# Optimization experiments

Hardware: AMD Instinct MI355X
Metric: run time of the kernel (lower is better)

The kernel has to match this reference:

```python
import jax, jax.numpy as jnp
import numpy as np

B, S, H = 1, 2048, 4096
NH, NKV, HD = 32, 8, 128
GROUPS = NH // NKV  # 4
THETA = 10000.0
NEG = -1e9


def setup_inputs() -> dict:
    key = jax.random.key(0)
    k1, k2, k3 = jax.random.split(key, 3)
    hidden_states = jax.random.normal(k1, (B, S, H), dtype=jnp.float32)
    w_qkv = jax.random.normal(k2, (H, (NH + 2 * NKV) * HD), dtype=jnp.float32) * 0.02
    w_o = jax.random.normal(k3, (NH * HD, H), dtype=jnp.float32) * 0.02
    causal = jnp.tril(jnp.ones((S, S), dtype=bool))
    attention_mask = jnp.where(causal, 0.0, NEG).astype(jnp.float32)[None, None]  # [1,1,S,S]
    return {"hidden_states": hidden_states, "w_qkv": w_qkv, "w_o": w_o,
            "attention_mask": attention_mask}


def _rope_freqs(seqlen, head_dim, theta):
    inv = 1.0 / (theta ** (jnp.arange(0, head_dim, 2, dtype=jnp.float32) / head_dim))
    t = jnp.arange(seqlen, dtype=jnp.float32)
    freqs = t[:, None] * inv[None, :]              # [S, HD/2]
    return jnp.cos(freqs), jnp.sin(freqs)


def _apply_rope(x, cos, sin):
    # x: [B,S,heads,HD]; source pairs x[i] with x[i+HD/2] (NeoX rotate-half)
    half = x.shape[-1] // 2
    x1, x2 = x[..., :half], x[..., half:]
    c = cos[None, :, None, :]
    s = sin[None, :, None, :]
    return jnp.concatenate([x1 * c - x2 * s, x1 * s + x2 * c], axis=-1)


def reference(hidden_states, w_qkv, w_o, attention_mask):
    bsz, seqlen, _ = hidden_states.shape
    xqkv = hidden_states @ w_qkv                            # [B,S,(NH+2*NKV)*HD]
    xqkv = xqkv.reshape(bsz, seqlen, NH + 2 * NKV, HD)
    xq = xqkv[:, :, :NH]                                    # [B,S,NH,HD]
    xk = xqkv[:, :, NH:NH + NKV]                            # [B,S,NKV,HD]
    xv = xqkv[:, :, NH + NKV:]                              # [B,S,NKV,HD]

    cos, sin = _rope_freqs(seqlen, HD, THETA)               # start_pos = 0 (prefill)
    xq = _apply_rope(xq, cos, sin)
    xk = _apply_rope(xk, cos, sin)

    # GQA: repeat kv heads to match query heads
    keys = jnp.repeat(xk, GROUPS, axis=2)                   # [B,S,NH,HD]
    values = jnp.repeat(xv, GROUPS, axis=2)

    scores = jnp.einsum('bqhd,bkhd->bhqk', xq, keys) / np.sqrt(HD)
    scores = scores + attention_mask
    probs = jax.nn.softmax(scores.astype(jnp.float32), axis=-1).astype(xq.dtype)
    out = jnp.einsum('bhqk,bkhd->bqhd', probs, values)      # [B,S,NH,HD]
    attention_weight = out.reshape(bsz, seqlen, NH * HD)
    attn_output = attention_weight @ w_o                    # [B,S,H]
    return attn_output
```

## Files before the change

kernel.cpp:

```cpp
#include <hip/hip_runtime.h>

typedef __bf16 bf16_8 __attribute__((ext_vector_type(8)));
typedef float f32x4 __attribute__((ext_vector_type(4)));
typedef unsigned short ushort8v __attribute__((ext_vector_type(8)));
typedef unsigned short ushort4v __attribute__((ext_vector_type(4)));

#define SEQ 2048
#define HDIM 4096
#define NHEADS 32
#define NKVH 8
#define HEADD 128
#define NQKV 6144

__device__ __forceinline__ unsigned short f2bf(float f) {
    unsigned int u = __float_as_uint(f);
    u += 0x7fffu + ((u >> 16) & 1u);
    return (unsigned short)(u >> 16);
}
__device__ __forceinline__ float bf2f(unsigned short v) {
    return __uint_as_float(((unsigned int)v) << 16);
}

#if defined(__has_builtin)
#if __has_builtin(__builtin_amdgcn_exp2f)
#define EXP2(x) __builtin_amdgcn_exp2f(x)
#endif
#endif
#ifndef EXP2
#define EXP2(x) __expf(0.69314718055994531f * (x))
#endif

typedef __attribute__((address_space(1))) void as1_void;
typedef __attribute__((address_space(3))) void as3_void;
__device__ __forceinline__ void gload16(const unsigned short* g, unsigned short* l) {
    __builtin_amdgcn_global_load_lds((as1_void*)g, (as3_void*)l, 16, 0, 0);
}

__global__ void k_f32_to_bf16(const float* __restrict__ in, unsigned short* __restrict__ out, int n) {
    int i = (blockIdx.x * blockDim.x + threadIdx.x) * 4;
    if (i >= n) return;
    float4 v = *reinterpret_cast<const float4*>(in + i);
    ushort4v o = { f2bf(v.x), f2bf(v.y), f2bf(v.z), f2bf(v.w) };
    *reinterpret_cast<ushort4v*>(out + i) = o;
}

__global__ void k_transpose_f32_to_bf16(const float* __restrict__ in, unsigned short* __restrict__ out,
                                        int K, int N) {
    __shared__ unsigned short tile[64][72];
    int k0 = blockIdx.y * 64, n0 = blockIdx.x * 64;
    int t = threadIdx.x;
    int r = t >> 2;
    int cs = (t & 3) * 16;
    int sw = (r >> 4) * 16;
    const float* src = in + (size_t)(k0 + r) * N + n0 + cs;
#pragma unroll
    for (int j = 0; j < 16; j += 4) {
        float4 v = *reinterpret_cast<const float4*>(src + j);
        tile[r][(cs + j + 0) ^ sw] = f2bf(v.x);
        tile[r][(cs + j + 1) ^ sw] = f2bf(v.y);
        tile[r][(cs + j + 2) ^ sw] = f2bf(v.z);
        tile[r][(cs + j + 3) ^ sw] = f2bf(v.w);
    }
    __syncthreads();
    int rr = t >> 2;
    int ks = (t & 3) * 16;
    unsigned short tmp[16];
#pragma unroll
    for (int i = 0; i < 16; i++) tmp[i] = tile[ks + i][rr ^ (((ks + i) >> 4) * 16)];
    unsigned short* dst = out + (size_t)(n0 + rr) * K + k0 + ks;
    *reinterpret_cast<ushort8v*>(dst) = *reinterpret_cast<const ushort8v*>(tmp);
    *reinterpret_cast<ushort8v*>(dst + 8) = *reinterpret_cast<const ushort8v*>(tmp + 8);
}

__global__ void k_transpose_bf16(const unsigned short* __restrict__ in, unsigned short* __restrict__ out,
                                 int inStride, int outStride) {
    __shared__ unsigned short tile[64][72];
    int r0 = blockIdx.y * 64, c0 = blockIdx.x * 64;
    int t = threadIdx.x;
    int r = t >> 2;
    int cs = (t & 3) * 16;
    int csw = cs ^ ((r >> 4) * 16);
    const unsigned short* src = in + (size_t)(r0 + r) * inStride + c0 + cs;
    *reinterpret_cast<ushort8v*>(&tile[r][csw])     = *reinterpret_cast<const ushort8v*>(src);
    *reinterpret_cast<ushort8v*>(&tile[r][csw + 8]) = *reinterpret_cast<const ushort8v*>(src + 8);
    __syncthreads();
    int rr = t >> 2;
    int ks = (t & 3) * 16;
    unsigned short tmp[16];
#pragma unroll
    for (int i = 0; i < 16; i++) tmp[i] = tile[ks + i][rr ^ (((ks + i) >> 4) * 16)];
    unsigned short* dst = out + (size_t)(c0 + rr) * outStride + r0 + ks;
    *reinterpret_cast<ushort8v*>(dst) = *reinterpret_cast<const ushort8v*>(tmp);
    *reinterpret_cast<ushort8v*>(dst + 8) = *reinterpret_cast<const ushort8v*>(tmp + 8);
}

template <bool OUT_BF16>
__global__ __launch_bounds__(256, 3) void k_gemm_bf16(
    const unsigned short* __restrict__ A,
    const unsigned short* __restrict__ Bt,
    void* __restrict__ Cv,
    int M, int N, int K)
{
    __shared__ unsigned short As[128 * 32];
    __shared__ unsigned short Bs[128 * 32];
    int m0 = blockIdx.y * 128, n0 = blockIdx.x * 128;
    int t = threadIdx.x;
    int w = t >> 6;
    int lane = t & 63;
    int l15 = lane & 15;
    int quad = lane >> 4;
    int wm = (w & 1) * 64, wn = (w >> 1) * 64;

    f32x4 acc[4][4] = {};

    int srow = w * 32 + (lane >> 2);
    int scol = (lane & 3) * 8;
    const unsigned short* aG = A + (size_t)(m0 + srow) * K + scol;
    const unsigned short* bG = Bt + (size_t)(n0 + srow) * K + scol;
    unsigned short* aL0 = &As[(w * 32) * 32];
    unsigned short* aL1 = &As[(w * 32 + 16) * 32];
    unsigned short* bL0 = &Bs[(w * 32) * 32];
    unsigned short* bL1 = &Bs[(w * 32 + 16) * 32];
    const size_t kstep16 = (size_t)16 * K;

    for (int k0 = 0; k0 < K; k0 += 32) {
        gload16(aG + k0, aL0);
        gload16(aG + k0 + kstep16, aL1);
        gload16(bG + k0, bL0);
        gload16(bG + k0 + kstep16, bL1);
        __syncthreads();

        bf16_8 af[4], bfr[4];
#pragma unroll
        for (int i = 0; i < 4; i++)
            af[i] = *reinterpret_cast<const bf16_8*>(&As[(wm + i * 16 + l15) * 32 + quad * 8]);
#pragma unroll
        for (int j = 0; j < 4; j++)
            bfr[j] = *reinterpret_cast<const bf16_8*>(&Bs[(wn + j * 16 + l15) * 32 + quad * 8]);
#pragma unroll
        for (int i = 0; i < 4; i++)
#pragma unroll
            for (int j = 0; j < 4; j++)
                acc[i][j] = __builtin_amdgcn_mfma_f32_16x16x32_bf16(af[i], bfr[j], acc[i][j], 0, 0, 0);
        __syncthreads();
    }

#pragma unroll
    for (int i = 0; i < 4; i++) {
        int row0 = m0 + wm + i * 16 + quad * 4;
#pragma unroll
        for (int j = 0; j < 4; j++) {
            int col = n0 + wn + j * 16 + l15;
#pragma unroll
            for (int r = 0; r < 4; r++) {
                float v = acc[i][j][r];
                if (OUT_BF16)
                    reinterpret_cast<unsigned short*>(Cv)[(size_t)(row0 + r) * N + col] = f2bf(v);
                else
                    reinterpret_cast<float*>(Cv)[(size_t)(row0 + r) * N + col] = v;
            }
        }
    }
}

__global__ void k_rope_split(const unsigned short* __restrict__ qkv,
                             unsigned short* __restrict__ Qb,
                             unsigned short* __restrict__ Kb)
{
    int wid = blockIdx.x * 4 + (threadIdx.x >> 6);
    int lane = threadIdx.x & 63;
    int head = wid % 40;
    int s = wid / 40;
    const unsigned short* src = qkv + (size_t)s * NQKV + head * HEADD;
    float x1 = bf2f(src[lane]);
    float x2 = bf2f(src[lane + 64]);
    float inv = __expf(-(float)lane * 0.14391156831212787f);
    float ang = (float)s * inv;
    float sn, c;
    __sincosf(ang, &sn, &c);
    float o1 = x1 * c - x2 * sn;
    float o2 = x1 * sn + x2 * c;
    unsigned short* dst;
    if (head < 32) {
        const float s2 = 0.12752908270648427f;
        o1 *= s2; o2 *= s2;
        dst = Qb + ((size_t)head * SEQ + s) * HEADD;
    } else {
        dst = Kb + ((size_t)(head - 32) * SEQ + s) * HEADD;
    }
    dst[lane] = f2bf(o1);
    dst[lane + 64] = f2bf(o2);
}

__global__ __launch_bounds__(256, 4) void k_attention(
    const unsigned short* __restrict__ Qb,
    const unsigned short* __restrict__ Kb,
    const unsigned short* __restrict__ Vt,
    unsigned short* __restrict__ Ob)
{
    __shared__ unsigned short Ks[64][136];
    __shared__ unsigned short Vs[128][72];
    __shared__ unsigned short Ps[4][16][72];
    int h  = blockIdx.y;
    int hkv = h >> 2;
    int t = threadIdx.x;
    int w = t >> 6, lane = t & 63, l15 = lane & 15, quad = lane >> 4;

    const unsigned short* kbase = Kb + (size_t)hkv * SEQ * HEADD;
    const unsigned short* vbase = Vt + (size_t)hkv * HEADD * SEQ;

    int qtile[2] = { (int)blockIdx.x, 31 - (int)blockIdx.x };

    for (int ph = 0; ph < 2; ph++) {
        int q0 = qtile[ph] * 64;
        int qm0 = q0 + w * 16;
        int qg = qm0 + l15;

        bf16_8 aq[4];
        {
            const unsigned short* qp = Qb + ((size_t)h * SEQ + qg) * HEADD + quad * 8;
#pragma unroll
            for (int kk = 0; kk < 4; kk++)
                aq[kk] = *reinterpret_cast<const bf16_8*>(qp + kk * 32);
        }

        f32x4 o[8] = {};
        float l_ = 0.f;

        for (int kv0 = 0; kv0 < q0 + 64; kv0 += 64) {
            __syncthreads();
#pragma unroll
            for (int p = 0; p < 4; p++) {
                int r = p * 16 + (t >> 4), c = (t & 15) * 8;
                *reinterpret_cast<ushort8v*>(&Ks[r][c]) =
                    *reinterpret_cast<const ushort8v*>(kbase + (size_t)(kv0 + r) * HEADD + c);
            }
#pragma unroll
            for (int p = 0; p < 4; p++) {
                int r = p * 32 + (t >> 3), c = (t & 7) * 8;
                *reinterpret_cast<ushort8v*>(&Vs[r][c]) =
                    *reinterpret_cast<const ushort8v*>(vbase + (size_t)r * SEQ + kv0 + c);
            }
            __syncthreads();

            if (kv0 > qm0 + 15) continue;

            f32x4 sc[4];
#pragma unroll
            for (int nt = 0; nt < 4; nt++) {
                f32x4 z = {};
#pragma unroll
                for (int kk = 0; kk < 4; kk++) {
                    bf16_8 bk = *reinterpret_cast<const bf16_8*>(&Ks[nt * 16 + l15][kk * 32 + quad * 8]);
                    z = __builtin_amdgcn_mfma_f32_16x16x32_bf16(bk, aq[kk], z, 0, 0, 0);
                }
                sc[nt] = z;
            }
            bool needMask = (kv0 + 63 > qm0);
#pragma unroll
            for (int nt = 0; nt < 4; nt++)
#pragma unroll
                for (int r = 0; r < 4; r++) {
                    float a = sc[nt][r] - 12.0f;
                    if (needMask) {
                        int kg = kv0 + nt * 16 + quad * 4 + r;
                        if (kg > qg) a = -1000.0f;
                    }
                    float p = EXP2(a);
                    sc[nt][r] = p;
                    l_ += p;
                }
#pragma unroll
            for (int nt = 0; nt < 4; nt++) {
                ushort4v pk = { f2bf(sc[nt][0]), f2bf(sc[nt][1]), f2bf(sc[nt][2]), f2bf(sc[nt][3]) };
                *reinterpret_cast<ushort4v*>(&Ps[w][l15][nt * 16 + quad * 4]) = pk;
            }
            asm volatile("s_waitcnt lgkmcnt(0)" ::: "memory");
            bf16_8 pf[2];
#pragma unroll
            for (int kk = 0; kk < 2; kk++)
                pf[kk] = *reinterpret_cast<const bf16_8*>(&Ps[w][l15][kk * 32 + quad * 8]);
#pragma unroll
            for (int dt = 0; dt < 8; dt++)
#pragma unroll
                for (int kk = 0; kk < 2; kk++) {
                    bf16_8 av = *reinterpret_cast<const bf16_8*>(&Vs[dt * 16 + l15][kk * 32 + quad * 8]);
                    o[dt] = __builtin_amdgcn_mfma_f32_16x16x32_bf16(av, pf[kk], o[dt], 0, 0, 0);
                }
        }
        l_ += __shfl_xor(l_, 16, 64);
        l_ += __shfl_xor(l_, 32, 64);
        float rinv = 1.0f / l_;
        unsigned short* orow = Ob + (size_t)qg * (NHEADS * HEADD) + h * HEADD + quad * 4;
#pragma unroll
        for (int dt = 0; dt < 8; dt++) {
            ushort4v pk = { f2bf(o[dt][0] * rinv), f2bf(o[dt][1] * rinv),
                            f2bf(o[dt][2] * rinv), f2bf(o[dt][3] * rinv) };
            *reinterpret_cast<ushort4v*>(orow + dt * 16) = pk;
        }
    }
}

extern "C" void kernel_launch(void* const* d_in, const int* in_sizes, int n_in,
                              void* d_out, int out_size, void* d_ws, size_t ws_size,
                              hipStream_t stream) {
    const float* hs    = (const float*)d_in[0];
    const float* w_qkv = (const float*)d_in[1];
    const float* w_o   = (const float*)d_in[2];

    char* ws = (char*)d_ws;
    size_t off = 0;
    auto alloc = [&](size_t bytes) -> void* {
        void* p = ws + off;
        off += (bytes + 255) & ~(size_t)255;
        return p;
    };
    unsigned short* Xb    = (unsigned short*)alloc((size_t)SEQ * HDIM * 2);
    unsigned short* R1    = (unsigned short*)alloc((size_t)NQKV * HDIM * 2);
    unsigned short* Wot   = (unsigned short*)alloc((size_t)HDIM * HDIM * 2);
    unsigned short* QKVb  = (unsigned short*)alloc((size_t)SEQ * NQKV * 2);
    unsigned short* Wqkvt = R1;
    unsigned short* Qb = R1;
    unsigned short* Kb = Qb + (size_t)NHEADS * SEQ * HEADD;
    unsigned short* Vt = Kb + (size_t)NKVH * SEQ * HEADD;
    unsigned short* AOb = Xb;

    k_f32_to_bf16<<<(SEQ * HDIM) / 1024, 256, 0, stream>>>(hs, Xb, SEQ * HDIM);
    k_transpose_f32_to_bf16<<<dim3(NQKV / 64, HDIM / 64), 256, 0, stream>>>(w_qkv, Wqkvt, HDIM, NQKV);
    k_transpose_f32_to_bf16<<<dim3(HDIM / 64, HDIM / 64), 256, 0, stream>>>(w_o, Wot, HDIM, HDIM);
    k_gemm_bf16<true><<<dim3(NQKV / 128, SEQ / 128), 256, 0, stream>>>(Xb, Wqkvt, QKVb, SEQ, NQKV, HDIM);
    k_rope_split<<<(SEQ * 40) / 4, 256, 0, stream>>>(QKVb, Qb, Kb);
    k_transpose_bf16<<<dim3((NKVH * HEADD) / 64, SEQ / 64), 256, 0, stream>>>(
        QKVb + (size_t)(NHEADS + NKVH) * HEADD, Vt, NQKV, SEQ);
    k_attention<<<dim3(16, NHEADS), 256, 0, stream>>>(Qb, Kb, Vt, AOb);
    k_gemm_bf16<false><<<dim3(HDIM / 128, SEQ / 128), 256, 0, stream>>>(AOb, Wot, d_out, SEQ, HDIM, HDIM);
}
```

Measured before the change: 527.7 us.

## Replace GEMM with 256x256-tile, double-buffered, swizzled-LDS pipelined kernel

Both projection GEMMs move from a 128x128 tile with single-buffered 32-wide K steps to a 256x256 tile over 512 threads with 64-wide K tiles. The K tiles are double-buffered in 128 KB of dynamic LDS, and a phased schedule overlaps global-to-LDS loads with MFMA work. LDS columns are XOR-swizzled to avoid bank conflicts, and block IDs are remapped so neighbouring blocks are grouped for L2 locality. The larger tile raises arithmetic intensity and hides load latency, but it lowers occupancy and leaves fewer blocks (192 and 128) for the machine's compute units, which could cause wave-quantization loss.

After: 546.7 us. +3.6%, slower.

```diff
diff --git a/kernel.cpp b/kernel.cpp
--- a/kernel.cpp
+++ b/kernel.cpp
@@ -94,74 +94,141 @@
     *reinterpret_cast<ushort8v*>(dst + 8) = *reinterpret_cast<const ushort8v*>(tmp + 8);
 }
 
+
+#define STAGE_A(TILE, KH) do { if ((TILE) < NT) {                                        \
+    size_t kb_ = (size_t)(TILE) * 128 + (size_t)((KH) * 64);                             \
+    gload16((const unsigned short*)(srcA0 + kb_),                                        \
+            (unsigned short*)(smem + ((TILE) & 1) * 32768 + (KH) * 16384 + wby));        \
+    gload16((const unsigned short*)(srcA1 + kb_),                                        \
+            (unsigned short*)(smem + ((TILE) & 1) * 32768 + (KH) * 16384 + 8192 + wby)); \
+  } } while (0)
+
+#define STAGE_B(TILE, KH) do { if ((TILE) < NT) {                                        \
+    size_t kb_ = (size_t)(TILE) * 128 + (size_t)((KH) * 64);                             \
+    gload16((const unsigned short*)(srcB0 + kb_),                                        \
+            (unsigned short*)(smem + 65536 + ((TILE) & 1) * 32768 + (KH) * 16384 + wby)); \
+    gload16((const unsigned short*)(srcB1 + kb_),                                        \
+            (unsigned short*)(smem + 65536 + ((TILE) & 1) * 32768 + (KH) * 16384 + 8192 + wby)); \
+  } } while (0)
+
+#define MFMA_ROW(ACCI, AV)                                                                \
+    acc[ACCI][0] = __builtin_amdgcn_mfma_f32_16x16x32_bf16(AV, b0, acc[ACCI][0], 0, 0, 0); \
+    acc[ACCI][1] = __builtin_amdgcn_mfma_f32_16x16x32_bf16(AV, b1, acc[ACCI][1], 0, 0, 0); \
+    acc[ACCI][2] = __builtin_amdgcn_mfma_f32_16x16x32_bf16(AV, b2, acc[ACCI][2], 0, 0, 0); \
+    acc[ACCI][3] = __builtin_amdgcn_mfma_f32_16x16x32_bf16(AV, b3, acc[ACCI][3], 0, 0, 0);
+
+#define PHASE(PB, PKH, PMH, DOB, STAGE_STMT, DOVM) do {                                   \
+    const char* ab_ = smem + (PB) * 32768 + (PKH) * 16384;                                \
+    a0 = *(const bf16_8*)(ab_ + offA[(PMH) * 4 + 0]);                                     \
+    a1 = *(const bf16_8*)(ab_ + offA[(PMH) * 4 + 1]);                                     \
+    a2 = *(const bf16_8*)(ab_ + offA[(PMH) * 4 + 2]);                                     \
+    a3 = *(const bf16_8*)(ab_ + offA[(PMH) * 4 + 3]);                                     \
+    if (DOB) {                                                                            \
+        const char* bb_ = smem + 65536 + (PB) * 32768 + (PKH) * 16384;                    \
+        b0 = *(const bf16_8*)(bb_ + offB[0]);                                             \
+        b1 = *(const bf16_8*)(bb_ + offB[1]);                                             \
+        b2 = *(const bf16_8*)(bb_ + offB[2]);                                             \
+        b3 = *(const bf16_8*)(bb_ + offB[3]);                                             \
+    }                                                                                     \
+    STAGE_STMT;                                                                           \
+    if (DOVM) asm volatile("s_waitcnt vmcnt(8)" ::: "memory");                            \
+    __builtin_amdgcn_s_barrier();                                                         \
+    __builtin_amdgcn_s_setprio(1);                                                        \
+    MFMA_ROW((PMH) * 4 + 0, a0)                                                           \
+    MFMA_ROW((PMH) * 4 + 1, a1)                                                           \
+    MFMA_ROW((PMH) * 4 + 2, a2)                                                           \
+    MFMA_ROW((PMH) * 4 + 3, a3)                                                           \
+    __builtin_amdgcn_s_setprio(0);                                                        \
+    asm volatile("s_waitcnt lgkmcnt(0)" ::: "memory");                                    \
+    __builtin_amdgcn_s_barrier();                                                         \
+  } while (0)
+
 template <bool OUT_BF16>
-__global__ __launch_bounds__(256, 3) void k_gemm_bf16(
+__global__ __launch_bounds__(512, 2) void k_gemm256(
     const unsigned short* __restrict__ A,
     const unsigned short* __restrict__ Bt,
     void* __restrict__ Cv,
-    int M, int N, int K)
+    int N, int K)
 {
-    __shared__ unsigned short As[128 * 32];
-    __shared__ unsigned short Bs[128 * 32];
-    int m0 = blockIdx.y * 128, n0 = blockIdx.x * 128;
+    extern __shared__ char smem[];
+    const int NT = K >> 6;
+    const int NTN = N >> 8;
+
+    int nwg = gridDim.x;
+    int bid = blockIdx.x;
+    int cpx = nwg >> 3;
+    int sw = (bid & 7) * cpx + (bid >> 3);
+    int tm = sw / NTN, tn = sw % NTN;
+    int gm0 = tm << 8, gn0 = tn << 8;
+
     int t = threadIdx.x;
-    int w = t >> 6;
-    int lane = t & 63;
-    int l15 = lane & 15;
-    int quad = lane >> 4;
-    int wm = (w & 1) * 64, wn = (w >> 1) * 64;
-
-    f32x4 acc[4][4] = {};
-
-    int srow = w * 32 + (lane >> 2);
-    int scol = (lane & 3) * 8;
-    const unsigned short* aG = A + (size_t)(m0 + srow) * K + scol;
-    const unsigned short* bG = Bt + (size_t)(n0 + srow) * K + scol;
-    unsigned short* aL0 = &As[(w * 32) * 32];
-    unsigned short* aL1 = &As[(w * 32 + 16) * 32];
-    unsigned short* bL0 = &Bs[(w * 32) * 32];
-    unsigned short* bL1 = &Bs[(w * 32 + 16) * 32];
-    const size_t kstep16 = (size_t)16 * K;
-
-    for (int k0 = 0; k0 < K; k0 += 32) {
-        gload16(aG + k0, aL0);
-        gload16(aG + k0 + kstep16, aL1);
-        gload16(bG + k0, bL0);
-        gload16(bG + k0 + kstep16, bL1);
-        __syncthreads();
-
-        bf16_8 af[4], bfr[4];
-#pragma unroll
-        for (int i = 0; i < 4; i++)
-            af[i] = *reinterpret_cast<const bf16_8*>(&As[(wm + i * 16 + l15) * 32 + quad * 8]);
-#pragma unroll
-        for (int j = 0; j < 4; j++)
-            bfr[j] = *reinterpret_cast<const bf16_8*>(&Bs[(wn + j * 16 + l15) * 32 + quad * 8]);
-#pragma unroll
-        for (int i = 0; i < 4; i++)
-#pragma unroll
-            for (int j = 0; j < 4; j++)
-                acc[i][j] = __builtin_amdgcn_mfma_f32_16x16x32_bf16(af[i], bfr[j], acc[i][j], 0, 0, 0);
-        __syncthreads();
-    }
-
-#pragma unroll
-    for (int i = 0; i < 4; i++) {
-        int row0 = m0 + wm + i * 16 + quad * 4;
-#pragma unroll
-        for (int j = 0; j < 4; j++) {
-            int col = n0 + wn + j * 16 + l15;
+    int w = t >> 6, lane = t & 63;
+    int l15 = lane & 15, quad = lane >> 4;
+    int wr = w >> 2, wc = w & 3;
+    int wby = w << 10;
+
+    int offA[8], offB[4];
+#pragma unroll
+    for (int mh = 0; mh < 2; mh++)
+#pragma unroll
+        for (int mi = 0; mi < 4; mi++) {
+            int row = wr * 128 + mh * 64 + mi * 16 + l15;
+            offA[mh * 4 + mi] = row * 64 + ((quad ^ ((row >> 1) & 3)) << 4);
+        }
+#pragma unroll
+    for (int nj = 0; nj < 4; nj++) {
+        int row = wc * 64 + nj * 16 + l15;
+        offB[nj] = row * 64 + ((quad ^ ((row >> 1) & 3)) << 4);
+    }
+
+    int srow0 = t >> 2;
+    int sslot = (t & 3) ^ ((srow0 >> 1) & 3);
+    const char* srcA0 = (const char*)A  + ((size_t)(gm0 + srow0)       * K + sslot * 8) * 2;
+    const char* srcA1 = (const char*)A  + ((size_t)(gm0 + srow0 + 128) * K + sslot * 8) * 2;
+    const char* srcB0 = (const char*)Bt + ((size_t)(gn0 + srow0)       * K + sslot * 8) * 2;
+    const char* srcB1 = (const char*)Bt + ((size_t)(gn0 + srow0 + 128) * K + sslot * 8) * 2;
+
+    f32x4 acc[8][4] = {};
+    bf16_8 a0, a1, a2, a3, b0, b1, b2, b3;
+
+    STAGE_A(0, 0); STAGE_B(0, 0);
+    STAGE_A(0, 1); STAGE_B(0, 1);
+    STAGE_A(1, 0); STAGE_B(1, 0);
+    asm volatile("s_waitcnt vmcnt(8)" ::: "memory");
+    __builtin_amdgcn_s_barrier();
+
+    const int NITER = K >> 7;
+    for (int it = 0; it < NITER; ++it) {
+        int T1 = 2 * it + 1, T2 = T1 + 1, T3 = T1 + 2;
+        PHASE(0, 0, 0, 1, STAGE_A(T1, 1), 0);
+        PHASE(0, 0, 1, 0, STAGE_B(T1, 1), 1);
+        PHASE(0, 1, 0, 1, STAGE_A(T2, 0), 0);
+        PHASE(0, 1, 1, 0, STAGE_B(T2, 0), 1);
+        PHASE(1, 0, 0, 1, STAGE_A(T2, 1), 0);
+        PHASE(1, 0, 1, 0, STAGE_B(T2, 1), 1);
+        PHASE(1, 1, 0, 1, STAGE_A(T3, 0), 0);
+        PHASE(1, 1, 1, 0, STAGE_B(T3, 0), 1);
+    }
+
+    int crow = gm0 + wr * 128 + quad * 4;
+    int ccol = gn0 + wc * 64 + l15;
+#pragma unroll
+    for (int m8 = 0; m8 < 8; m8++)
+#pragma unroll
+        for (int nj = 0; nj < 4; nj++)
 #pragma unroll
             for (int r = 0; r < 4; r++) {
-                float v = acc[i][j][r];
-                if (OUT_BF16)
-                    reinterpret_cast<unsigned short*>(Cv)[(size_t)(row0 + r) * N + col] = f2bf(v);
-                else
-                    reinterpret_cast<float*>(Cv)[(size_t)(row0 + r) * N + col] = v;
+                size_t idx = (size_t)(crow + m8 * 16 + r) * N + (ccol + nj * 16);
+                float v = acc[m8][nj][r];
+                if (OUT_BF16) ((unsigned short*)Cv)[idx] = f2bf(v);
+                else          ((float*)Cv)[idx] = v;
             }
-        }
-    }
-}
+}
+
+#undef STAGE_A
+#undef STAGE_B
+#undef MFMA_ROW
+#undef PHASE
 
 __global__ void k_rope_split(const unsigned short* __restrict__ qkv,
                              unsigned short* __restrict__ Qb,
@@ -308,6 +375,15 @@
     const float* w_qkv = (const float*)d_in[1];
     const float* w_o   = (const float*)d_in[2];
 
+    static bool s_attr_set = false;
+    if (!s_attr_set) {
+        hipFuncSetAttribute(reinterpret_cast<const void*>(k_gemm256<true>),
+                            hipFuncAttributeMaxDynamicSharedMemorySize, 131072);
+        hipFuncSetAttribute(reinterpret_cast<const void*>(k_gemm256<false>),
+                            hipFuncAttributeMaxDynamicSharedMemorySize, 131072);
+        s_attr_set = true;
+    }
+
     char* ws = (char*)d_ws;
     size_t off = 0;
     auto alloc = [&](size_t bytes) -> void* {
@@ -328,10 +404,12 @@
     k_f32_to_bf16<<<(SEQ * HDIM) / 1024, 256, 0, stream>>>(hs, Xb, SEQ * HDIM);
     k_transpose_f32_to_bf16<<<dim3(NQKV / 64, HDIM / 64), 256, 0, stream>>>(w_qkv, Wqkvt, HDIM, NQKV);
     k_transpose_f32_to_bf16<<<dim3(HDIM / 64, HDIM / 64), 256, 0, stream>>>(w_o, Wot, HDIM, HDIM);
-    k_gemm_bf16<true><<<dim3(NQKV / 128, SEQ / 128), 256, 0, stream>>>(Xb, Wqkvt, QKVb, SEQ, NQKV, HDIM);
+    k_gemm256<true><<<dim3((SEQ / 256) * (NQKV / 256)), dim3(512), 131072, stream>>>(
+        Xb, Wqkvt, QKVb, NQKV, HDIM);
     k_rope_split<<<(SEQ * 40) / 4, 256, 0, stream>>>(QKVb, Qb, Kb);
     k_transpose_bf16<<<dim3((NKVH * HEADD) / 64, SEQ / 64), 256, 0, stream>>>(
         QKVb + (size_t)(NHEADS + NKVH) * HEADD, Vt, NQKV, SEQ);
     k_attention<<<dim3(16, NHEADS), 256, 0, stream>>>(Qb, Kb, Vt, AOb);
-    k_gemm_bf16<false><<<dim3(HDIM / 128, SEQ / 128), 256, 0, stream>>>(AOb, Wot, d_out, SEQ, HDIM, HDIM);
-}
+    k_gemm256<false><<<dim3((SEQ / 256) * (HDIM / 256)), dim3(512), 131072, stream>>>(
+        AOb, Wot, d_out, HDIM, HDIM);
+}
```
